# Kernel tuning notes

Hardware: AMD Instinct MI355X
Metric: run time of the kernel (lower is better)

Reference implementation:

```python
import jax, jax.numpy as jnp
import numpy as np

N_NODES = 50000
N_EDGES = 800000
VOCAB = 4096
EMB = 128
HID = 128


def glorot(key, shape):
    limit = float(np.sqrt(6.0 / (shape[0] + shape[1])))
    return jax.random.uniform(key, shape, jnp.float32, -limit, limit)


def setup_inputs() -> dict:
    key = jax.random.key(0)
    k = jax.random.split(key, 6)
    x = jax.random.randint(k[0], (N_NODES, 1), 0, VOCAB, dtype=jnp.int64)
    edge_index = jax.random.randint(k[1], (2, N_EDGES), 0, N_NODES, dtype=jnp.int64)
    # Embedding init: normal(0, dim^-0.5)
    emb = jax.random.normal(k[2], (VOCAB, EMB), jnp.float32) * (EMB ** -0.5)
    W1 = glorot(k[3], (EMB, 2 * HID))
    b1 = jnp.zeros((2 * HID,), jnp.float32)
    W2 = glorot(k[4], (2 * HID, HID))
    b2 = jnp.zeros((HID,), jnp.float32)
    return {"x": x, "edge_index": edge_index, "emb": emb,
            "W1": W1, "b1": b1, "W2": W2, "b2": b2}


def _gcn_conv(h, src, dst, norm, W, b):
    # PyG GCNConv: transform then degree-normalized aggregate over A + I.
    h = h @ W                                   # [N, F_out]
    msg = norm[:, None] * h[src]                # [(E+N), F_out] gather
    out = jax.ops.segment_sum(msg, dst, num_segments=N_NODES)  # scatter-add
    return out + b


def _edges_with_self_loops_and_norm(edge_index):
    loop = jnp.arange(N_NODES, dtype=edge_index.dtype)
    src = jnp.concatenate([edge_index[0], loop])
    dst = jnp.concatenate([edge_index[1], loop])
    deg = jax.ops.segment_sum(jnp.ones_like(dst, jnp.float32), dst,
                              num_segments=N_NODES)
    inv_sqrt = jnp.where(deg > 0, deg ** -0.5, 0.0)
    norm = inv_sqrt[src] * inv_sqrt[dst]        # [(E+N)]
    return src, dst, norm


def reference(x, edge_index, emb, W1, b1, W2, b2):
    src, dst, norm = _edges_with_self_loops_and_norm(edge_index)
    h = emb[x[:, 0]]                            # embedding lookup + squeeze(1)
    h = jax.nn.relu(_gcn_conv(h, src, dst, norm, W1, b1))
    h = _gcn_conv(h, src, dst, norm, W2, b2)
    return h
```

## Files before the change

kernel.cpp:

```cpp
#include <hip/hip_runtime.h>


constexpr int FEAT = 128;
constexpr int HID2 = 256;
constexpr int CAP  = 64;

typedef __attribute__((ext_vector_type(8))) __bf16 bf16x8;
typedef __attribute__((ext_vector_type(4))) float f32x4;
union FragU { uint4 u; bf16x8 b; };

__device__ inline void split_bf16_rne(float v, unsigned short& h, unsigned short& l) {
  unsigned u = __float_as_uint(v);
  unsigned short hh = (unsigned short)((u + 0x7FFFu + ((u >> 16) & 1u)) >> 16);
  float r = v - __uint_as_float(((unsigned)hh) << 16);
  unsigned u2 = __float_as_uint(r);
  unsigned short ll = (unsigned short)((u2 + 0x7FFFu + ((u2 >> 16) & 1u)) >> 16);
  h = hh; l = ll;
}

__device__ inline void split_trunc1(float v, unsigned short& h, unsigned short& l) {
  unsigned u = __float_as_uint(v);
  h = (unsigned short)(u >> 16);
  float r = v - __uint_as_float(u & 0xFFFF0000u);
  l = (unsigned short)(__float_as_uint(r) >> 16);
}


__global__ __launch_bounds__(256) void k_init_prep(int* cnt, int N, int nblkN,
    const float* __restrict__ W1, const float* __restrict__ W2,
    unsigned short* __restrict__ w1s_hi, unsigned short* __restrict__ w1s_lo,
    unsigned short* __restrict__ w2s_hi, unsigned short* __restrict__ w2s_lo) {
  int b = blockIdx.x;
  if (b < nblkN) {
    int i = b * 256 + threadIdx.x;
    if (i < N) cnt[i] = 0;
    return;
  }
  int idx = (b - nblkN) * 256 + threadIdx.x;
  unsigned short h, l;
  if (idx < FEAT * HID2) {
    int k = idx >> 8, n = idx & 255;
    split_bf16_rne(W1[idx], h, l);
    int t = n >> 4, lr = n & 15, kc = k >> 5, quad = (k >> 3) & 3, j = k & 7;
    int us = (((t * 4 + kc) * 64 + quad * 16 + lr) << 3) + j;
    w1s_hi[us] = h;
    w1s_lo[us] = l;
  } else {
    int jj = idx - FEAT * HID2;
    int k = jj >> 7, n = jj & 127;
    split_bf16_rne(W2[jj], h, l);
    int t = n >> 4, lr = n & 15, kc = k >> 5, quad = (k >> 3) & 3, j = k & 7;
    int us = (((t * 8 + kc) * 64 + quad * 16 + lr) << 3) + j;
    w2s_hi[us] = h;
    w2s_lo[us] = l;
  }
}


__global__ __launch_bounds__(256) void k_bucket(const int* __restrict__ src,
    const int* __restrict__ dst, int* cnt, int* csr, int E, int chunkN) {
  int g = blockIdx.x & 7;
  int e = (blockIdx.x >> 3) * 256 + threadIdx.x;
  if (e >= E) return;
  int d = dst[e];
  int lo = g * chunkN;
  if (d >= lo && d < lo + chunkN) {
    int pos = atomicAdd(&cnt[d], 1);
    if (pos < CAP) csr[d * CAP + pos] = src[e];
  }
}

__global__ __launch_bounds__(256) void k_inv_sqrt(const int* __restrict__ cnt,
                                                  float* invs, int N) {
  int i = blockIdx.x * 256 + threadIdx.x;
  if (i < N) invs[i] = rsqrtf((float)(cnt[i] + 1));
}


__global__ __launch_bounds__(256) void k_gather_l1(const int* __restrict__ x,
    const float* __restrict__ emb, const int* __restrict__ cnt,
    const int* __restrict__ csr, const float* __restrict__ invs,
    unsigned short* __restrict__ aggf_hi, unsigned short* __restrict__ aggf_lo,
    int N) {
  int half  = blockIdx.x & 1;
  int chunk = blockIdx.x >> 1;
  int node  = chunk * 16 + (threadIdx.x >> 4);
  if (node >= N) return;
  int c4 = half * 64 + (threadIdx.x & 15) * 4;
  float wd = invs[node];

  float4 acc = *reinterpret_cast<const float4*>(&emb[(long long)x[node] * FEAT + c4]);
  acc.x *= wd; acc.y *= wd; acc.z *= wd; acc.w *= wd;

  const int* row = csr + node * CAP;
  int deg = cnt[node];
  if (deg > CAP) deg = CAP;
  int j = 0;
  for (; j + 3 < deg; j += 4) {
    int s0 = row[j], s1 = row[j + 1], s2 = row[j + 2], s3 = row[j + 3];
    float w0 = invs[s0], w1 = invs[s1], w2 = invs[s2], w3 = invs[s3];
    float4 a = *reinterpret_cast<const float4*>(&emb[(long long)x[s0] * FEAT + c4]);
    float4 b = *reinterpret_cast<const float4*>(&emb[(long long)x[s1] * FEAT + c4]);
    float4 c = *reinterpret_cast<const float4*>(&emb[(long long)x[s2] * FEAT + c4]);
    float4 d = *reinterpret_cast<const float4*>(&emb[(long long)x[s3] * FEAT + c4]);
    acc.x += w0 * a.x + w1 * b.x + w2 * c.x + w3 * d.x;
    acc.y += w0 * a.y + w1 * b.y + w2 * c.y + w3 * d.y;
    acc.z += w0 * a.z + w1 * b.z + w2 * c.z + w3 * d.z;
    acc.w += w0 * a.w + w1 * b.w + w2 * c.w + w3 * d.w;
  }
  for (; j < deg; ++j) {
    int s = row[j];
    float w = invs[s];
    float4 a = *reinterpret_cast<const float4*>(&emb[(long long)x[s] * FEAT + c4]);
    acc.x += w * a.x; acc.y += w * a.y; acc.z += w * a.z; acc.w += w * a.w;
  }

  acc.x *= wd; acc.y *= wd; acc.z *= wd; acc.w *= wd;
  ushort4 h4, l4;
  split_bf16_rne(acc.x, h4.x, l4.x);
  split_bf16_rne(acc.y, h4.y, l4.y);
  split_bf16_rne(acc.z, h4.z, l4.z);
  split_bf16_rne(acc.w, h4.w, l4.w);

  int T = node >> 4, lr = node & 15;
  int kc = c4 >> 5, quad = (c4 >> 3) & 3, sub = c4 & 7;
  long long us = (((long long)(T * 4 + kc) * 64 + quad * 16 + lr) << 3) + sub;
  *reinterpret_cast<ushort4*>(aggf_hi + us) = h4;
  *reinterpret_cast<ushort4*>(aggf_lo + us) = l4;
}


__global__ __launch_bounds__(256) void k_gather_l2(const float* __restrict__ hs2s,
    const int* __restrict__ cnt, const int* __restrict__ csr,
    const float* __restrict__ invs, const float* __restrict__ bias,
    float* __restrict__ out, int N, int Np) {
  int slice = blockIdx.x & 7;
  int chunk = blockIdx.x >> 3;
  int node  = chunk * 64 + (threadIdx.x >> 2);
  if (node >= N) return;
  int sc4 = (threadIdx.x & 3) * 4;
  const float* sl = hs2s + (long long)slice * Np * 16;

  float4 acc = *reinterpret_cast<const float4*>(&sl[node * 16 + sc4]);
  const int* row = csr + node * CAP;
  int deg = cnt[node];
  if (deg > CAP) deg = CAP;
  int j = 0;
  for (; j + 7 < deg; j += 8) {
    float4 r[8];
    #pragma unroll
    for (int q = 0; q < 8; ++q)
      r[q] = *reinterpret_cast<const float4*>(&sl[row[j + q] * 16 + sc4]);
    #pragma unroll
    for (int q = 0; q < 8; ++q) {
      acc.x += r[q].x; acc.y += r[q].y; acc.z += r[q].z; acc.w += r[q].w;
    }
  }
  if (j + 3 < deg) {
    float4 r[4];
    #pragma unroll
    for (int q = 0; q < 4; ++q)
      r[q] = *reinterpret_cast<const float4*>(&sl[row[j + q] * 16 + sc4]);
    #pragma unroll
    for (int q = 0; q < 4; ++q) {
      acc.x += r[q].x; acc.y += r[q].y; acc.z += r[q].z; acc.w += r[q].w;
    }
    j += 4;
  }
  for (; j < deg; ++j) {
    float4 a = *reinterpret_cast<const float4*>(&sl[row[j] * 16 + sc4]);
    acc.x += a.x; acc.y += a.y; acc.z += a.z; acc.w += a.w;
  }

  float w = invs[node];
  int col = slice * 16 + sc4;
  float4 b = *reinterpret_cast<const float4*>(&bias[col]);
  acc.x = acc.x * w + b.x; acc.y = acc.y * w + b.y;
  acc.z = acc.z * w + b.z; acc.w = acc.w * w + b.w;
  *reinterpret_cast<float4*>(&out[(long long)node * FEAT + col]) = acc;
}


__global__ __launch_bounds__(256, 2) void k_mlp(
    const uint4* __restrict__ aggf_hi, const uint4* __restrict__ aggf_lo,
    const uint4* __restrict__ w1s_hi, const uint4* __restrict__ w1s_lo,
    const uint4* __restrict__ w2s_hi, const uint4* __restrict__ w2s_lo,
    const float* __restrict__ b1, const float* __restrict__ invs,
    float* __restrict__ hs2s, int N, int Np) {
  __shared__ __align__(16) unsigned short h1h[32 * 256];
  __shared__ __align__(16) unsigned short h1l[32 * 256];

  int tid  = threadIdx.x;
  int wave = tid >> 6, lane = tid & 63, quad = lane >> 4, lr = lane & 15;
  int m0 = blockIdx.x * 32;
  int Tb = blockIdx.x * 2;

  FragU a1h[2][4], a1l[2][4];
  #pragma unroll
  for (int rt = 0; rt < 2; ++rt)
    #pragma unroll
    for (int kc = 0; kc < 4; ++kc) {
      a1h[rt][kc].u = aggf_hi[(long long)((Tb + rt) * 4 + kc) * 64 + lane];
      a1l[rt][kc].u = aggf_lo[(long long)((Tb + rt) * 4 + kc) * 64 + lane];
    }

  FragU bh[2][4], bl[2][4];
  auto loadB1 = [&](int t, int buf) {
    #pragma unroll
    for (int kc = 0; kc < 4; ++kc) {
      bh[buf][kc].u = w1s_hi[(t * 4 + kc) * 64 + lane];
      bl[buf][kc].u = w1s_lo[(t * 4 + kc) * 64 + lane];
    }
  };
  auto comp1 = [&](int t, int buf) {
    f32x4 hh[2], hl[2], lh[2];
    #pragma unroll
    for (int rt = 0; rt < 2; ++rt) {
      hh[rt] = f32x4{0.f, 0.f, 0.f, 0.f};
      hl[rt] = f32x4{0.f, 0.f, 0.f, 0.f};
      lh[rt] = f32x4{0.f, 0.f, 0.f, 0.f};
    }
    #pragma unroll
    for (int kc = 0; kc < 4; ++kc)
      #pragma unroll
      for (int rt = 0; rt < 2; ++rt) {
        hh[rt] = __builtin_amdgcn_mfma_f32_16x16x32_bf16(a1h[rt][kc].b, bh[buf][kc].b, hh[rt], 0, 0, 0);
        hl[rt] = __builtin_amdgcn_mfma_f32_16x16x32_bf16(a1h[rt][kc].b, bl[buf][kc].b, hl[rt], 0, 0, 0);
        lh[rt] = __builtin_amdgcn_mfma_f32_16x16x32_bf16(a1l[rt][kc].b, bh[buf][kc].b, lh[rt], 0, 0, 0);
      }
    float bias = b1[t * 16 + lr];
    int c = t * 2 + (lr >> 3), jj = lr & 7;
    #pragma unroll
    for (int rt = 0; rt < 2; ++rt)
      #pragma unroll
      for (int r = 0; r < 4; ++r) {
        float v = hh[rt][r] + hl[rt][r] + lh[rt][r] + bias;
        v = v > 0.f ? v : 0.f;
        int row = rt * 16 + quad * 4 + r;
        int us = ((row * 32 + (c ^ (row & 7))) << 3) + jj;
        unsigned short sh, sl;
        split_trunc1(v, sh, sl);
        h1h[us] = sh;
        h1l[us] = sl;
      }
  };

  int t0 = wave * 4;
  loadB1(t0, 0);
  #pragma unroll
  for (int i = 0; i < 4; ++i) {
    if (i < 3) loadB1(t0 + i + 1, (i + 1) & 1);
    comp1(t0 + i, i & 1);
  }

  __syncthreads();

  float inv_r[2][4];
  #pragma unroll
  for (int rt = 0; rt < 2; ++rt)
    #pragma unroll
    for (int r = 0; r < 4; ++r) {
      int g = m0 + rt * 16 + quad * 4 + r;
      inv_r[rt][r] = invs[g < N ? g : N - 1];
    }

  #pragma unroll
  for (int ti = 0; ti < 2; ++ti) {
    int t2 = wave * 2 + ti;
    f32x4 hh[2], hl[2], lh[2];
    #pragma unroll
    for (int rt = 0; rt < 2; ++rt) {
      hh[rt] = f32x4{0.f, 0.f, 0.f, 0.f};
      hl[rt] = f32x4{0.f, 0.f, 0.f, 0.f};
      lh[rt] = f32x4{0.f, 0.f, 0.f, 0.f};
    }
    #pragma unroll
    for (int kh = 0; kh < 2; ++kh) {
      FragU b2h[4], b2l[4];
      #pragma unroll
      for (int kc = 0; kc < 4; ++kc) {
        b2h[kc].u = w2s_hi[(t2 * 8 + kh * 4 + kc) * 64 + lane];
        b2l[kc].u = w2s_lo[(t2 * 8 + kh * 4 + kc) * 64 + lane];
      }
      FragU a2h[2][4], a2l[2][4];
      #pragma unroll
      for (int rt = 0; rt < 2; ++rt) {
        int row = rt * 16 + lr;
        #pragma unroll
        for (int kc = 0; kc < 4; ++kc) {
          int pc = (kh * 16 + kc * 4 + quad) ^ (row & 7);
          a2h[rt][kc].u = *reinterpret_cast<const uint4*>(&h1h[(row * 32 + pc) << 3]);
          a2l[rt][kc].u = *reinterpret_cast<const uint4*>(&h1l[(row * 32 + pc) << 3]);
        }
      }
      #pragma unroll
      for (int kc = 0; kc < 4; ++kc)
        #pragma unroll
        for (int rt = 0; rt < 2; ++rt) {
          hh[rt] = __builtin_amdgcn_mfma_f32_16x16x32_bf16(a2h[rt][kc].b, b2h[kc].b, hh[rt], 0, 0, 0);
          hl[rt] = __builtin_amdgcn_mfma_f32_16x16x32_bf16(a2h[rt][kc].b, b2l[kc].b, hl[rt], 0, 0, 0);
          lh[rt] = __builtin_amdgcn_mfma_f32_16x16x32_bf16(a2l[rt][kc].b, b2h[kc].b, lh[rt], 0, 0, 0);
        }
    }
    float* sl = hs2s + (long long)t2 * Np * 16;
    #pragma unroll
    for (int rt = 0; rt < 2; ++rt)
      #pragma unroll
      for (int r = 0; r < 4; ++r) {
        int g = m0 + rt * 16 + quad * 4 + r;
        if (g < N)
          sl[g * 16 + lr] = (hh[rt][r] + hl[rt][r] + lh[rt][r]) * inv_r[rt][r];
      }
  }
}


extern "C" void kernel_launch(void* const* d_in, const int* in_sizes, int n_in,
                              void* d_out, int out_size, void* d_ws, size_t ws_size,
                              hipStream_t stream) {
  const int*   x   = (const int*)d_in[0];
  const int*   ei  = (const int*)d_in[1];
  const float* emb = (const float*)d_in[2];
  const float* W1  = (const float*)d_in[3];
  const float* b1  = (const float*)d_in[4];
  const float* W2  = (const float*)d_in[5];
  const float* b2  = (const float*)d_in[6];
  float* out = (float*)d_out;

  const int N  = in_sizes[0];
  const int E  = in_sizes[1] / 2;
  const int nblk_mlp = (N + 31) / 32;
  const int Np = nblk_mlp * 32;
  const int chunkN = (N + 7) / 8;
  const int* src = ei;
  const int* dst = ei + E;

  int* cnt      = (int*)d_ws;
  int* csr      = cnt + N;
  float* invs   = (float*)(csr + (long long)N * CAP);
  unsigned short* aggf_hi = (unsigned short*)(invs + N);
  unsigned short* aggf_lo = aggf_hi + (long long)Np * FEAT;
  float* hs2s   = (float*)(aggf_lo + (long long)Np * FEAT);
  unsigned short* w1s_hi = (unsigned short*)(hs2s + (long long)Np * FEAT);
  unsigned short* w1s_lo = w1s_hi + FEAT * HID2;
  unsigned short* w2s_hi = w1s_lo + FEAT * HID2;
  unsigned short* w2s_lo = w2s_hi + FEAT * HID2;

  const int nblk_N  = (N + 255) / 256;
  const int nblk_E8 = ((E + 255) / 256) * 8;
  const int nblk_g1 = ((N + 15) / 16) * 2;
  const int nblk_g2 = ((N + 63) / 64) * 8;

  k_init_prep<<<nblk_N + 256, 256, 0, stream>>>(cnt, N, nblk_N, W1, W2,
                                                w1s_hi, w1s_lo, w2s_hi, w2s_lo);
  k_bucket<<<nblk_E8, 256, 0, stream>>>(src, dst, cnt, csr, E, chunkN);
  k_inv_sqrt<<<nblk_N, 256, 0, stream>>>(cnt, invs, N);

  k_gather_l1<<<nblk_g1, 256, 0, stream>>>(x, emb, cnt, csr, invs,
                                           aggf_hi, aggf_lo, N);
  k_mlp<<<nblk_mlp, 256, 0, stream>>>((const uint4*)aggf_hi, (const uint4*)aggf_lo,
                                      (const uint4*)w1s_hi, (const uint4*)w1s_lo,
                                      (const uint4*)w2s_hi, (const uint4*)w2s_lo,
                                      b1, invs, hs2s, N, Np);
  k_gather_l2<<<nblk_g2, 256, 0, stream>>>(hs2s, cnt, csr, invs, b2,
                                           out, N, Np);
}
```

Before: 242.8 us.

## Store CSR indices as 16-bit, recompute inverse sqrt degree inline

Bucketed neighbor lists are stored as unsigned short instead of int, halving CSR write and read traffic. The gather kernels load them eight or sixteen at a time with vector loads. The separate inverse-sqrt-degree kernel and its buffer are removed; every consumer recomputes rsqrt(cnt+1) from the degree counts. The layer-2 gather unroll also grows to 16 neighbors. The 16-bit indices only work while the node count stays below 65536, and recomputing rsqrt adds a little ALU work per neighbor.

```diff
diff --git a/kernel.cpp b/kernel.cpp
--- a/kernel.cpp
+++ b/kernel.cpp
@@ -58,7 +58,7 @@
 
 
 __global__ __launch_bounds__(256) void k_bucket(const int* __restrict__ src,
-    const int* __restrict__ dst, int* cnt, int* csr, int E, int chunkN) {
+    const int* __restrict__ dst, int* cnt, unsigned short* csr, int E, int chunkN) {
   int g = blockIdx.x & 7;
   int e = (blockIdx.x >> 3) * 256 + threadIdx.x;
   if (e >= E) return;
@@ -66,20 +66,14 @@
   int lo = g * chunkN;
   if (d >= lo && d < lo + chunkN) {
     int pos = atomicAdd(&cnt[d], 1);
-    if (pos < CAP) csr[d * CAP + pos] = src[e];
-  }
-}
-
-__global__ __launch_bounds__(256) void k_inv_sqrt(const int* __restrict__ cnt,
-                                                  float* invs, int N) {
-  int i = blockIdx.x * 256 + threadIdx.x;
-  if (i < N) invs[i] = rsqrtf((float)(cnt[i] + 1));
+    if (pos < CAP) csr[d * CAP + pos] = (unsigned short)src[e];
+  }
 }
 
 
 __global__ __launch_bounds__(256) void k_gather_l1(const int* __restrict__ x,
     const float* __restrict__ emb, const int* __restrict__ cnt,
-    const int* __restrict__ csr, const float* __restrict__ invs,
+    const unsigned short* __restrict__ csr,
     unsigned short* __restrict__ aggf_hi, unsigned short* __restrict__ aggf_lo,
     int N) {
   int half  = blockIdx.x & 1;
@@ -87,30 +81,61 @@
   int node  = chunk * 16 + (threadIdx.x >> 4);
   if (node >= N) return;
   int c4 = half * 64 + (threadIdx.x & 15) * 4;
-  float wd = invs[node];
+  int degN = cnt[node];
+  float wd = rsqrtf((float)(degN + 1));
+  int deg = degN > CAP ? CAP : degN;
 
   float4 acc = *reinterpret_cast<const float4*>(&emb[(long long)x[node] * FEAT + c4]);
   acc.x *= wd; acc.y *= wd; acc.z *= wd; acc.w *= wd;
 
-  const int* row = csr + node * CAP;
-  int deg = cnt[node];
-  if (deg > CAP) deg = CAP;
+  const unsigned short* row = csr + node * CAP;
   int j = 0;
-  for (; j + 3 < deg; j += 4) {
-    int s0 = row[j], s1 = row[j + 1], s2 = row[j + 2], s3 = row[j + 3];
-    float w0 = invs[s0], w1 = invs[s1], w2 = invs[s2], w3 = invs[s3];
-    float4 a = *reinterpret_cast<const float4*>(&emb[(long long)x[s0] * FEAT + c4]);
-    float4 b = *reinterpret_cast<const float4*>(&emb[(long long)x[s1] * FEAT + c4]);
-    float4 c = *reinterpret_cast<const float4*>(&emb[(long long)x[s2] * FEAT + c4]);
-    float4 d = *reinterpret_cast<const float4*>(&emb[(long long)x[s3] * FEAT + c4]);
-    acc.x += w0 * a.x + w1 * b.x + w2 * c.x + w3 * d.x;
-    acc.y += w0 * a.y + w1 * b.y + w2 * c.y + w3 * d.y;
-    acc.z += w0 * a.z + w1 * b.z + w2 * c.z + w3 * d.z;
-    acc.w += w0 * a.w + w1 * b.w + w2 * c.w + w3 * d.w;
+  for (; j + 7 < deg; j += 8) {
+    uint4 c8 = *reinterpret_cast<const uint4*>(row + j);
+    int s[8] = {(int)(c8.x & 0xFFFF), (int)(c8.x >> 16),
+                (int)(c8.y & 0xFFFF), (int)(c8.y >> 16),
+                (int)(c8.z & 0xFFFF), (int)(c8.z >> 16),
+                (int)(c8.w & 0xFFFF), (int)(c8.w >> 16)};
+    int xs[8];
+    float ws[8];
+    #pragma unroll
+    for (int q = 0; q < 8; ++q) xs[q] = x[s[q]];
+    #pragma unroll
+    for (int q = 0; q < 8; ++q) ws[q] = rsqrtf((float)(cnt[s[q]] + 1));
+    float4 r[8];
+    #pragma unroll
+    for (int q = 0; q < 8; ++q)
+      r[q] = *reinterpret_cast<const float4*>(&emb[(long long)xs[q] * FEAT + c4]);
+    #pragma unroll
+    for (int q = 0; q < 8; ++q) {
+      acc.x += ws[q] * r[q].x; acc.y += ws[q] * r[q].y;
+      acc.z += ws[q] * r[q].z; acc.w += ws[q] * r[q].w;
+    }
+  }
+  if (j + 3 < deg) {
+    uint2 c4e = *reinterpret_cast<const uint2*>(row + j);
+    int s[4] = {(int)(c4e.x & 0xFFFF), (int)(c4e.x >> 16),
+                (int)(c4e.y & 0xFFFF), (int)(c4e.y >> 16)};
+    int xs[4];
+    float ws[4];
+    #pragma unroll
+    for (int q = 0; q < 4; ++q) xs[q] = x[s[q]];
+    #pragma unroll
+    for (int q = 0; q < 4; ++q) ws[q] = rsqrtf((float)(cnt[s[q]] + 1));
+    float4 r[4];
+    #pragma unroll
+    for (int q = 0; q < 4; ++q)
+      r[q] = *reinterpret_cast<const float4*>(&emb[(long long)xs[q] * FEAT + c4]);
+    #pragma unroll
+    for (int q = 0; q < 4; ++q) {
+      acc.x += ws[q] * r[q].x; acc.y += ws[q] * r[q].y;
+      acc.z += ws[q] * r[q].z; acc.w += ws[q] * r[q].w;
+    }
+    j += 4;
   }
   for (; j < deg; ++j) {
     int s = row[j];
-    float w = invs[s];
+    float w = rsqrtf((float)(cnt[s] + 1));
     float4 a = *reinterpret_cast<const float4*>(&emb[(long long)x[s] * FEAT + c4]);
     acc.x += w * a.x; acc.y += w * a.y; acc.z += w * a.z; acc.w += w * a.w;
   }
@@ -131,9 +156,8 @@
 
 
 __global__ __launch_bounds__(256) void k_gather_l2(const float* __restrict__ hs2s,
-    const int* __restrict__ cnt, const int* __restrict__ csr,
-    const float* __restrict__ invs, const float* __restrict__ bias,
-    float* __restrict__ out, int N, int Np) {
+    const int* __restrict__ cnt, const unsigned short* __restrict__ csr,
+    const float* __restrict__ bias, float* __restrict__ out, int N, int Np) {
   int slice = blockIdx.x & 7;
   int chunk = blockIdx.x >> 3;
   int node  = chunk * 64 + (threadIdx.x >> 2);
@@ -142,25 +166,54 @@
   const float* sl = hs2s + (long long)slice * Np * 16;
 
   float4 acc = *reinterpret_cast<const float4*>(&sl[node * 16 + sc4]);
-  const int* row = csr + node * CAP;
-  int deg = cnt[node];
-  if (deg > CAP) deg = CAP;
+  const unsigned short* row = csr + node * CAP;
+  int degN = cnt[node];
+  int deg = degN > CAP ? CAP : degN;
   int j = 0;
-  for (; j + 7 < deg; j += 8) {
+  for (; j + 15 < deg; j += 16) {
+    uint4 c0 = *reinterpret_cast<const uint4*>(row + j);
+    uint4 c1 = *reinterpret_cast<const uint4*>(row + j + 8);
+    int s[16] = {(int)(c0.x & 0xFFFF), (int)(c0.x >> 16),
+                 (int)(c0.y & 0xFFFF), (int)(c0.y >> 16),
+                 (int)(c0.z & 0xFFFF), (int)(c0.z >> 16),
+                 (int)(c0.w & 0xFFFF), (int)(c0.w >> 16),
+                 (int)(c1.x & 0xFFFF), (int)(c1.x >> 16),
+                 (int)(c1.y & 0xFFFF), (int)(c1.y >> 16),
+                 (int)(c1.z & 0xFFFF), (int)(c1.z >> 16),
+                 (int)(c1.w & 0xFFFF), (int)(c1.w >> 16)};
+    float4 r[16];
+    #pragma unroll
+    for (int q = 0; q < 16; ++q)
+      r[q] = *reinterpret_cast<const float4*>(&sl[s[q] * 16 + sc4]);
+    #pragma unroll
+    for (int q = 0; q < 16; ++q) {
+      acc.x += r[q].x; acc.y += r[q].y; acc.z += r[q].z; acc.w += r[q].w;
+    }
+  }
+  if (j + 7 < deg) {
+    uint4 c8 = *reinterpret_cast<const uint4*>(row + j);
+    int s[8] = {(int)(c8.x & 0xFFFF), (int)(c8.x >> 16),
+                (int)(c8.y & 0xFFFF), (int)(c8.y >> 16),
+                (int)(c8.z & 0xFFFF), (int)(c8.z >> 16),
+                (int)(c8.w & 0xFFFF), (int)(c8.w >> 16)};
     float4 r[8];
     #pragma unroll
     for (int q = 0; q < 8; ++q)
-      r[q] = *reinterpret_cast<const float4*>(&sl[row[j + q] * 16 + sc4]);
+      r[q] = *reinterpret_cast<const float4*>(&sl[s[q] * 16 + sc4]);
     #pragma unroll
     for (int q = 0; q < 8; ++q) {
       acc.x += r[q].x; acc.y += r[q].y; acc.z += r[q].z; acc.w += r[q].w;
     }
+    j += 8;
   }
   if (j + 3 < deg) {
+    uint2 c4e = *reinterpret_cast<const uint2*>(row + j);
+    int s[4] = {(int)(c4e.x & 0xFFFF), (int)(c4e.x >> 16),
+                (int)(c4e.y & 0xFFFF), (int)(c4e.y >> 16)};
     float4 r[4];
     #pragma unroll
     for (int q = 0; q < 4; ++q)
-      r[q] = *reinterpret_cast<const float4*>(&sl[row[j + q] * 16 + sc4]);
+      r[q] = *reinterpret_cast<const float4*>(&sl[s[q] * 16 + sc4]);
     #pragma unroll
     for (int q = 0; q < 4; ++q) {
       acc.x += r[q].x; acc.y += r[q].y; acc.z += r[q].z; acc.w += r[q].w;
@@ -172,7 +225,7 @@
     acc.x += a.x; acc.y += a.y; acc.z += a.z; acc.w += a.w;
   }
 
-  float w = invs[node];
+  float w = rsqrtf((float)(degN + 1));
   int col = slice * 16 + sc4;
   float4 b = *reinterpret_cast<const float4*>(&bias[col]);
   acc.x = acc.x * w + b.x; acc.y = acc.y * w + b.y;
@@ -185,7 +238,7 @@
     const uint4* __restrict__ aggf_hi, const uint4* __restrict__ aggf_lo,
     const uint4* __restrict__ w1s_hi, const uint4* __restrict__ w1s_lo,
     const uint4* __restrict__ w2s_hi, const uint4* __restrict__ w2s_lo,
-    const float* __restrict__ b1, const float* __restrict__ invs,
+    const float* __restrict__ b1, const int* __restrict__ cnt,
     float* __restrict__ hs2s, int N, int Np) {
   __shared__ __align__(16) unsigned short h1h[32 * 256];
   __shared__ __align__(16) unsigned short h1l[32 * 256];
@@ -261,7 +314,7 @@
     #pragma unroll
     for (int r = 0; r < 4; ++r) {
       int g = m0 + rt * 16 + quad * 4 + r;
-      inv_r[rt][r] = invs[g < N ? g : N - 1];
+      inv_r[rt][r] = rsqrtf((float)(cnt[g < N ? g : N - 1] + 1));
     }
 
   #pragma unroll
@@ -335,10 +388,9 @@
   const int* src = ei;
   const int* dst = ei + E;
 
-  int* cnt      = (int*)d_ws;
-  int* csr      = cnt + N;
-  float* invs   = (float*)(csr + (long long)N * CAP);
-  unsigned short* aggf_hi = (unsigned short*)(invs + N);
+  int* cnt = (int*)d_ws;
+  unsigned short* csr = (unsigned short*)(cnt + N);
+  unsigned short* aggf_hi = csr + (long long)N * CAP;
   unsigned short* aggf_lo = aggf_hi + (long long)Np * FEAT;
   float* hs2s   = (float*)(aggf_lo + (long long)Np * FEAT);
   unsigned short* w1s_hi = (unsigned short*)(hs2s + (long long)Np * FEAT);
@@ -354,14 +406,12 @@
   k_init_prep<<<nblk_N + 256, 256, 0, stream>>>(cnt, N, nblk_N, W1, W2,
                                                 w1s_hi, w1s_lo, w2s_hi, w2s_lo);
   k_bucket<<<nblk_E8, 256, 0, stream>>>(src, dst, cnt, csr, E, chunkN);
-  k_inv_sqrt<<<nblk_N, 256, 0, stream>>>(cnt, invs, N);
-
-  k_gather_l1<<<nblk_g1, 256, 0, stream>>>(x, emb, cnt, csr, invs,
+
+  k_gather_l1<<<nblk_g1, 256, 0, stream>>>(x, emb, cnt, csr,
                                            aggf_hi, aggf_lo, N);
   k_mlp<<<nblk_mlp, 256, 0, stream>>>((const uint4*)aggf_hi, (const uint4*)aggf_lo,
                                       (const uint4*)w1s_hi, (const uint4*)w1s_lo,
                                       (const uint4*)w2s_hi, (const uint4*)w2s_lo,
-                                      b1, invs, hs2s, N, Np);
-  k_gather_l2<<<nblk_g2, 256, 0, stream>>>(hs2s, cnt, csr, invs, b2,
-                                           out, N, Np);
-}
+                                      b1, cnt, hs2s, N, Np);
+  k_gather_l2<<<nblk_g2, 256, 0, stream>>>(hs2s, cnt, csr, b2, out, N, Np);
+}
```

After: 237.6 us. -2.2%, faster.
